# Performance work log

Measured on AMD Instinct MI355X. Metric: run time of the kernel, lower is better.

The kernel has to match this reference:

```python
import jax, jax.numpy as jnp
import numpy as np
import math

DIM = 2048
N_PHASES = 8
B, L = 4, 4096


def setup_inputs() -> dict:
    key = jax.random.key(0)
    ks = jax.random.split(key, 12)
    s = 0.02
    return {
        "x": jax.random.normal(ks[0], (B, L, DIM), dtype=jnp.float32),
        # weights stored [in, out] (transposed vs torch Linear)
        "Wp": jax.random.normal(ks[1], (DIM, N_PHASES), dtype=jnp.float32) * s,
        "bp": jnp.zeros((N_PHASES,), dtype=jnp.float32),
        "Wa": jax.random.normal(ks[2], (DIM, N_PHASES), dtype=jnp.float32) * s,
        "ba": jnp.zeros((N_PHASES,), dtype=jnp.float32),
        "Wv": jax.random.normal(ks[3], (DIM, DIM), dtype=jnp.float32) * s,
        "bv": jnp.zeros((DIM,), dtype=jnp.float32),
        "ln_g": jnp.ones((DIM,), dtype=jnp.float32),
        "ln_b": jnp.zeros((DIM,), dtype=jnp.float32),
        "Wo": jax.random.normal(ks[4], (DIM, DIM), dtype=jnp.float32) * s,
        "bo": jnp.zeros((DIM,), dtype=jnp.float32),
    }


def _layernorm(h, g, b, eps=1e-5):
    mu = jnp.mean(h, axis=-1, keepdims=True)
    var = jnp.var(h, axis=-1, keepdims=True)
    return (h - mu) * jax.lax.rsqrt(var + eps) * g + b


def reference(x, Wp, bp, Wa, ba, Wv, bv, ln_g, ln_b, Wo, bo):
    Llen = x.shape[1]
    phase = jnp.tanh(x @ Wp + bp) * math.pi          # [B,L,P]
    amp = jax.nn.softplus(x @ Wa + ba) + 0.1         # [B,L,P]
    value = x @ Wv + bv                              # [B,L,D]
    # (value[...,None,:] * cos_p[...,None] * amp[...,None]).sum(-2)
    # == value * sum_p(cos_p * amp)  -- algebraic factorization, same math.
    cr = jnp.sum(jnp.cos(phase) * amp, axis=-1, keepdims=True)  # [B,L,1]
    ci = jnp.sum(jnp.sin(phase) * amp, axis=-1, keepdims=True)  # [B,L,1]
    bound = value * (cr + ci)                        # real+imag combined
    retrieved = jnp.cumsum(bound, axis=1)            # [B,L,D]
    h = _layernorm(retrieved / math.sqrt(Llen), ln_g, ln_b)
    return x + h @ Wo + bo
```

## Files before the change

kernel.cpp:

```cpp
#include <hip/hip_runtime.h>

#define DIM   2048
#define LSEQ  4096
#define BATCH 4
#define NTOK  (BATCH*LSEQ)
#define NCH   16
#define CHL   (LSEQ/NCH)
#define PI_F  3.14159265358979f
#define NT    (DIM/64)

typedef __bf16 bf16x8 __attribute__((ext_vector_type(8)));
typedef float  f32x4  __attribute__((ext_vector_type(4)));
typedef float  f32x8  __attribute__((ext_vector_type(8)));
typedef unsigned short ushort8 __attribute__((ext_vector_type(8)));

__device__ __forceinline__ unsigned short f2bf(float f) {
    unsigned int u = __float_as_uint(f);
    u += 0x7fffu + ((u >> 16) & 1u);
    return (unsigned short)(u >> 16);
}

__device__ __forceinline__ void gload_lds16(const void* g, void* l) {
    __builtin_amdgcn_global_load_lds(
        (const __attribute__((address_space(1))) void*)g,
        (__attribute__((address_space(3))) void*)l, 16, 0, 0);
}

__global__ __launch_bounds__(256) void k_transpose(const float* __restrict__ src,
                                                   unsigned short* __restrict__ dst) {
    __shared__ float tile[32][33];
    int tx = threadIdx.x, ty = threadIdx.y;
    int k0 = blockIdx.y * 32, n0 = blockIdx.x * 32;
#pragma unroll
    for (int r = 0; r < 4; r++)
        tile[ty + r * 8][tx] = src[(size_t)(k0 + ty + r * 8) * DIM + n0 + tx];
    __syncthreads();
#pragma unroll
    for (int r = 0; r < 4; r++)
        dst[(size_t)(n0 + ty + r * 8) * DIM + k0 + tx] = f2bf(tile[tx][ty + r * 8]);
}

__global__ __launch_bounds__(256) void k_prep_wpa(const float* __restrict__ Wp,
                                                  const float* __restrict__ Wa,
                                                  unsigned short* __restrict__ WpaT) {
    int idx = blockIdx.x * 256 + threadIdx.x;
    int p = idx >> 11, k = idx & (DIM - 1);
    float v = (p < 8) ? Wp[(size_t)k * 8 + p] : Wa[(size_t)k * 8 + (p - 8)];
    WpaT[idx] = f2bf(v);
}

__global__ __launch_bounds__(256) void k_sproj_mfma(const float* __restrict__ x,
                                                    const unsigned short* __restrict__ WpaT,
                                                    const float* __restrict__ bp,
                                                    const float* __restrict__ ba,
                                                    float* __restrict__ s,
                                                    unsigned short* __restrict__ xbf) {
    const int t = threadIdx.x;
    const int w = t >> 6, l = t & 63;
    const int r16 = l & 15, q = l >> 4;
    const int rowbase = blockIdx.x * 64 + w * 16;
    const float* xr = x + (size_t)(rowbase + r16) * DIM + q * 8;
    unsigned short* xw = xbf + (size_t)(rowbase + r16) * DIM + q * 8;
    const unsigned short* wrow = WpaT + r16 * DIM + q * 8;

    f32x4 acc = {};
#pragma unroll 8
    for (int ks = 0; ks < 64; ks++) {
        f32x8 xv = *(const f32x8*)(xr + ks * 32);
        ushort8 xo;
#pragma unroll
        for (int j = 0; j < 8; j++) xo[j] = f2bf(xv[j]);
        *(ushort8*)(xw + ks * 32) = xo;
        bf16x8 av = *(const bf16x8*)&xo;
        bf16x8 bv = *(const bf16x8*)(wrow + ks * 32);
        acc = __builtin_amdgcn_mfma_f32_16x16x32_bf16(av, bv, acc, 0, 0, 0);
    }
    const float bpv = bp[r16 & 7], bav = ba[r16 & 7];
#pragma unroll
    for (int j = 0; j < 4; j++) {
        float z = acc[j];
        float zo = __shfl_xor(z, 8);
        float zp = z + bpv, za = zo + bav;
        float ph = tanhf(zp) * PI_F;
        float amp = (za > 20.f ? za : log1pf(expf(za))) + 0.1f;
        float term = (r16 < 8) ? (cosf(ph) + sinf(ph)) * amp : 0.f;
        term += __shfl_xor(term, 1);
        term += __shfl_xor(term, 2);
        term += __shfl_xor(term, 4);
        if (r16 == 0) s[rowbase + q * 4 + j] = term;
    }
}

__device__ __forceinline__ void stage_unit(const unsigned short* __restrict__ src,
                                           unsigned short* dst, int tid) {
    gload_lds16(src,                     dst + tid * 8);
    gload_lds16(src + (size_t)128 * DIM, dst + (tid + 512) * 8);
}

template <int EPI>
__global__ __launch_bounds__(512, 2) void k_gemm256(const unsigned short* __restrict__ A,
                                                    const unsigned short* __restrict__ Bt,
                                                    const float* __restrict__ bias,
                                                    const float* __restrict__ sc,
                                                    const float* __restrict__ resid,
                                                    float* __restrict__ C,
                                                    float* __restrict__ part) {
    __shared__ __align__(16) unsigned short As[2][2][256 * 32];
    __shared__ __align__(16) unsigned short Bs[2][2][256 * 32];
    __shared__ float colsum[2][256];
    const int tid = threadIdx.x;
    const int w = tid >> 6, lane = tid & 63;
    const int wm = w >> 2, wn = w & 3;
    const int r16 = lane & 15, q = lane >> 4;

    int bid = blockIdx.x;
    int wgs = (bid & 7) * 64 + (bid >> 3);
    int tm = wgs >> 3, tn = wgs & 7;
    int brow = tm * 256, bcol = tn * 256;

    const int kq = ((tid & 3) ^ ((tid >> 3) & 3)) * 8;
    const unsigned short* pA = A  + (size_t)(brow + (tid >> 2)) * DIM + kq;
    const unsigned short* pB = Bt + (size_t)(bcol + (tid >> 2)) * DIM + kq;

    const int qs8 = (q ^ ((r16 >> 1) & 3)) * 8;
    const int offA = (wm * 128 + r16) * 32 + qs8;
    const int offB = (wn * 64  + r16) * 32 + qs8;

    f32x4 acc[8][4] = {};

    stage_unit(pA,      &As[0][0][0], tid);
    stage_unit(pB,      &Bs[0][0][0], tid);
    stage_unit(pA + 32, &As[0][1][0], tid);
    stage_unit(pB + 32, &Bs[0][1][0], tid);
    stage_unit(pA + 64, &As[1][0][0], tid);
    asm volatile("s_waitcnt vmcnt(6)" ::: "memory");
    __builtin_amdgcn_s_barrier();

    for (int t = 0; t < NT; ++t) {
        const int s = t & 1;
        unsigned short* A0 = &As[s][0][0];
        unsigned short* A1 = &As[s][1][0];
        unsigned short* B0 = &Bs[s][0][0];
        unsigned short* B1 = &Bs[s][1][0];
        unsigned short* nA1 = &As[s ^ 1][1][0];
        unsigned short* nB0 = &Bs[s ^ 1][0][0];
        unsigned short* nB1 = &Bs[s ^ 1][1][0];
        const unsigned short* pAn = pA + (t + 1) * 64;
        const unsigned short* pBn = pB + (t + 1) * 64;

        bf16x8 aF[4], bF[4];
#pragma unroll
        for (int i = 0; i < 4; i++) aF[i] = *(const bf16x8*)(A0 + offA + i * 512);
#pragma unroll
        for (int i = 0; i < 4; i++) bF[i] = *(const bf16x8*)(B0 + offB + i * 512);
        stage_unit(pBn, nB0, tid);
        __builtin_amdgcn_s_barrier();
        __builtin_amdgcn_s_setprio(1);
#pragma unroll
        for (int i = 0; i < 4; i++)
#pragma unroll
            for (int n = 0; n < 4; n++)
                acc[i][n] = __builtin_amdgcn_mfma_f32_16x16x32_bf16(aF[i], bF[n], acc[i][n], 0, 0, 0);
        __builtin_amdgcn_s_setprio(0);
        __builtin_amdgcn_s_barrier();

#pragma unroll
        for (int i = 0; i < 4; i++) aF[i] = *(const bf16x8*)(A0 + offA + 2048 + i * 512);
        stage_unit(pAn + 32, nA1, tid);
        __builtin_amdgcn_s_barrier();
        __builtin_amdgcn_s_setprio(1);
#pragma unroll
        for (int i = 0; i < 4; i++)
#pragma unroll
            for (int n = 0; n < 4; n++)
                acc[4 + i][n] = __builtin_amdgcn_mfma_f32_16x16x32_bf16(aF[i], bF[n], acc[4 + i][n], 0, 0, 0);
        __builtin_amdgcn_s_setprio(0);
        asm volatile("s_waitcnt vmcnt(6)" ::: "memory");
        __builtin_amdgcn_s_barrier();

#pragma unroll
        for (int i = 0; i < 4; i++) aF[i] = *(const bf16x8*)(A1 + offA + i * 512);
#pragma unroll
        for (int i = 0; i < 4; i++) bF[i] = *(const bf16x8*)(B1 + offB + i * 512);
        stage_unit(pBn + 32, nB1, tid);
        __builtin_amdgcn_s_barrier();
        __builtin_amdgcn_s_setprio(1);
#pragma unroll
        for (int i = 0; i < 4; i++)
#pragma unroll
            for (int n = 0; n < 4; n++)
                acc[i][n] = __builtin_amdgcn_mfma_f32_16x16x32_bf16(aF[i], bF[n], acc[i][n], 0, 0, 0);
        __builtin_amdgcn_s_setprio(0);
        __builtin_amdgcn_s_barrier();

#pragma unroll
        for (int i = 0; i < 4; i++) aF[i] = *(const bf16x8*)(A1 + offA + 2048 + i * 512);
        stage_unit(pA + (t + 2) * 64, A0, tid);
        __builtin_amdgcn_s_barrier();
        __builtin_amdgcn_s_setprio(1);
#pragma unroll
        for (int i = 0; i < 4; i++)
#pragma unroll
            for (int n = 0; n < 4; n++)
                acc[4 + i][n] = __builtin_amdgcn_mfma_f32_16x16x32_bf16(aF[i], bF[n], acc[4 + i][n], 0, 0, 0);
        __builtin_amdgcn_s_setprio(0);
        asm volatile("s_waitcnt vmcnt(6)" ::: "memory");
        __builtin_amdgcn_s_barrier();
    }

    float cs[4] = {0.f, 0.f, 0.f, 0.f};
#pragma unroll
    for (int mf = 0; mf < 8; mf++) {
        int r0 = brow + wm * 128 + mf * 16 + q * 4;
#pragma unroll
        for (int nf = 0; nf < 4; nf++) {
            int c = bcol + wn * 64 + nf * 16 + r16;
            float bc = bias[c];
#pragma unroll
            for (int j = 0; j < 4; j++) {
                int r = r0 + j;
                float v = acc[mf][nf][j] + bc;
                if (EPI == 0) { v *= sc[r]; cs[nf] += v; }
                else          v += resid[(size_t)r * DIM + c];
                C[(size_t)r * DIM + c] = v;
            }
        }
    }
    if (EPI == 0) {
#pragma unroll
        for (int nf = 0; nf < 4; nf++) {
            float v = cs[nf];
            v += __shfl_xor(v, 16);
            v += __shfl_xor(v, 32);
            if (q == 0) colsum[wm][wn * 64 + nf * 16 + r16] = v;
        }
        __syncthreads();
        if (tid < 256)
            part[(size_t)(brow >> 8) * DIM + bcol + tid] = colsum[0][tid] + colsum[1][tid];
    }
}

__global__ __launch_bounds__(256) void k_scan_offsets(float* __restrict__ part) {
    int tid = blockIdx.x * 256 + threadIdx.x;
    int d = tid & (DIM - 1);
    int b = tid >> 11;
    float run = 0.f;
    for (int ch = 0; ch < NCH; ch++) {
        size_t idx = ((size_t)b * NCH + ch) * DIM + d;
        float v = part[idx];
        part[idx] = run;
        run += v;
    }
}

__global__ __launch_bounds__(256) void k_scan_apply(float* __restrict__ bound,
                                                    const float* __restrict__ part) {
    int tid = blockIdx.x * 256 + threadIdx.x;
    int d = tid & (DIM - 1);
    int ch = (tid >> 11) & (NCH - 1);
    int b = tid >> 15;
    float run = part[tid];
    float* p = bound + ((size_t)b * LSEQ + (size_t)ch * CHL) * DIM + d;
    for (int i = 0; i < CHL; i++) { run += p[(size_t)i * DIM]; p[(size_t)i * DIM] = run; }
}

__global__ __launch_bounds__(256) void k_lnorm(const float* __restrict__ ret,
                                               const float* __restrict__ g,
                                               const float* __restrict__ bta,
                                               unsigned short* __restrict__ h) {
    int row = blockIdx.x, t = threadIdx.x;
    const float4* r4 = (const float4*)(ret + (size_t)row * DIM);
    float4 v0 = r4[2 * t], v1 = r4[2 * t + 1];
    const float scl = 1.0f / 64.0f;
    v0.x *= scl; v0.y *= scl; v0.z *= scl; v0.w *= scl;
    v1.x *= scl; v1.y *= scl; v1.z *= scl; v1.w *= scl;
    float sum = v0.x + v0.y + v0.z + v0.w + v1.x + v1.y + v1.z + v1.w;
    float ss  = v0.x*v0.x + v0.y*v0.y + v0.z*v0.z + v0.w*v0.w
              + v1.x*v1.x + v1.y*v1.y + v1.z*v1.z + v1.w*v1.w;
#pragma unroll
    for (int off = 32; off; off >>= 1) { sum += __shfl_down(sum, off); ss += __shfl_down(ss, off); }
    __shared__ float red[4][2];
    __shared__ float mu_s, rstd_s;
    int w = t >> 6, lane = t & 63;
    if (lane == 0) { red[w][0] = sum; red[w][1] = ss; }
    __syncthreads();
    if (t == 0) {
        float S = red[0][0] + red[1][0] + red[2][0] + red[3][0];
        float Q = red[0][1] + red[1][1] + red[2][1] + red[3][1];
        float mu = S / DIM;
        float var = Q / DIM - mu * mu;
        mu_s = mu; rstd_s = rsqrtf(var + 1e-5f);
    }
    __syncthreads();
    float mu = mu_s, rstd = rstd_s;
    f32x8 gv = *(const f32x8*)(g + t * 8);
    f32x8 bv = *(const f32x8*)(bta + t * 8);
    float vv[8] = { v0.x, v0.y, v0.z, v0.w, v1.x, v1.y, v1.z, v1.w };
    ushort8 o;
#pragma unroll
    for (int j = 0; j < 8; j++) o[j] = f2bf((vv[j] - mu) * rstd * gv[j] + bv[j]);
    *(ushort8*)(h + (size_t)row * DIM + t * 8) = o;
}

extern "C" void kernel_launch(void* const* d_in, const int* in_sizes, int n_in,
                              void* d_out, int out_size, void* d_ws, size_t ws_size,
                              hipStream_t stream) {
    const float* x   = (const float*)d_in[0];
    const float* Wp  = (const float*)d_in[1];
    const float* bp  = (const float*)d_in[2];
    const float* Wa  = (const float*)d_in[3];
    const float* ba  = (const float*)d_in[4];
    const float* Wv  = (const float*)d_in[5];
    const float* bv  = (const float*)d_in[6];
    const float* lng = (const float*)d_in[7];
    const float* lnb = (const float*)d_in[8];
    const float* Wo  = (const float*)d_in[9];
    const float* bo  = (const float*)d_in[10];
    float* out = (float*)d_out;

    char* ws = (char*)d_ws;
    unsigned short* x_bf = (unsigned short*)ws; ws += (size_t)NTOK * DIM * 2;
    unsigned short* WvT  = (unsigned short*)ws; ws += (size_t)DIM * DIM * 2;
    unsigned short* WoT  = (unsigned short*)ws; ws += (size_t)DIM * DIM * 2;
    unsigned short* WpaT = (unsigned short*)ws; ws += (size_t)16 * DIM * 2;
    float* svec          = (float*)ws;          ws += (size_t)NTOK * 4;
    float* bound         = (float*)ws;          ws += (size_t)NTOK * DIM * 4;
    float* part          = (float*)ws;          ws += (size_t)BATCH * NCH * DIM * 4;

    dim3 tb(32, 8);
    k_transpose<<<dim3(64, 64), tb, 0, stream>>>(Wv, WvT);
    k_transpose<<<dim3(64, 64), tb, 0, stream>>>(Wo, WoT);
    k_prep_wpa<<<128, 256, 0, stream>>>(Wp, Wa, WpaT);
    k_sproj_mfma<<<NTOK / 64, 256, 0, stream>>>(x, WpaT, bp, ba, svec, x_bf);

    k_gemm256<0><<<512, 512, 0, stream>>>(x_bf, WvT, bv, svec, nullptr, bound, part);

    k_scan_offsets<<<BATCH * DIM / 256, 256, 0, stream>>>(part);
    k_scan_apply<<<BATCH * NCH * DIM / 256, 256, 0, stream>>>(bound, part);

    k_lnorm<<<NTOK, 256, 0, stream>>>(bound, lng, lnb, x_bf);

    k_gemm256<1><<<512, 512, 0, stream>>>(x_bf, WoT, bo, nullptr, x, out, nullptr);
}
```

Measured before the change: 433.5 us.

## Restructure GEMM main loop into two phases with fewer barriers

The bf16 MFMA GEMM main loop goes from four sub-phases, each with two barriers, to two phases per k-tile. Each phase loads all 8 A fragments and 4 B fragments, issues two staging loads, runs 32 MFMAs, then waits with vmcnt(4) and hits a single barrier. The aim is to cut barrier count and synchronisation stalls while giving the scheduler larger MFMA blocks, plus unroll-by-2 of the loop. In exchange it holds more fragment registers, which may lower occupancy, and the changed staging order and wait counts raise the risk of LDS read/write races.

```diff
diff --git a/kernel.cpp b/kernel.cpp
--- a/kernel.cpp
+++ b/kernel.cpp
@@ -136,75 +136,41 @@
     asm volatile("s_waitcnt vmcnt(6)" ::: "memory");
     __builtin_amdgcn_s_barrier();
 
+#pragma unroll 2
     for (int t = 0; t < NT; ++t) {
         const int s = t & 1;
-        unsigned short* A0 = &As[s][0][0];
-        unsigned short* A1 = &As[s][1][0];
-        unsigned short* B0 = &Bs[s][0][0];
-        unsigned short* B1 = &Bs[s][1][0];
-        unsigned short* nA1 = &As[s ^ 1][1][0];
-        unsigned short* nB0 = &Bs[s ^ 1][0][0];
-        unsigned short* nB1 = &Bs[s ^ 1][1][0];
-        const unsigned short* pAn = pA + (t + 1) * 64;
-        const unsigned short* pBn = pB + (t + 1) * 64;
-
-        bf16x8 aF[4], bF[4];
-#pragma unroll
-        for (int i = 0; i < 4; i++) aF[i] = *(const bf16x8*)(A0 + offA + i * 512);
-#pragma unroll
-        for (int i = 0; i < 4; i++) bF[i] = *(const bf16x8*)(B0 + offB + i * 512);
-        stage_unit(pBn, nB0, tid);
-        __builtin_amdgcn_s_barrier();
+        bf16x8 aF[8], bF[4];
+
+#pragma unroll
+        for (int i = 0; i < 8; i++) aF[i] = *(const bf16x8*)(&As[s][0][0] + offA + i * 512);
+#pragma unroll
+        for (int n = 0; n < 4; n++) bF[n] = *(const bf16x8*)(&Bs[s][0][0] + offB + n * 512);
+        stage_unit(pB + (t + 1) * 64,      &Bs[s ^ 1][0][0], tid);
+        stage_unit(pA + (t + 1) * 64 + 32, &As[s ^ 1][1][0], tid);
         __builtin_amdgcn_s_setprio(1);
 #pragma unroll
-        for (int i = 0; i < 4; i++)
+        for (int i = 0; i < 8; i++)
 #pragma unroll
             for (int n = 0; n < 4; n++)
                 acc[i][n] = __builtin_amdgcn_mfma_f32_16x16x32_bf16(aF[i], bF[n], acc[i][n], 0, 0, 0);
         __builtin_amdgcn_s_setprio(0);
+        asm volatile("s_waitcnt vmcnt(4)" ::: "memory");
         __builtin_amdgcn_s_barrier();
 
 #pragma unroll
-        for (int i = 0; i < 4; i++) aF[i] = *(const bf16x8*)(A0 + offA + 2048 + i * 512);
-        stage_unit(pAn + 32, nA1, tid);
-        __builtin_amdgcn_s_barrier();
+        for (int i = 0; i < 8; i++) aF[i] = *(const bf16x8*)(&As[s][1][0] + offA + i * 512);
+#pragma unroll
+        for (int n = 0; n < 4; n++) bF[n] = *(const bf16x8*)(&Bs[s][1][0] + offB + n * 512);
+        stage_unit(pB + (t + 1) * 64 + 32, &Bs[s ^ 1][1][0], tid);
+        stage_unit(pA + (t + 2) * 64,      &As[s][0][0], tid);
         __builtin_amdgcn_s_setprio(1);
 #pragma unroll
-        for (int i = 0; i < 4; i++)
-#pragma unroll
-            for (int n = 0; n < 4; n++)
-                acc[4 + i][n] = __builtin_amdgcn_mfma_f32_16x16x32_bf16(aF[i], bF[n], acc[4 + i][n], 0, 0, 0);
-        __builtin_amdgcn_s_setprio(0);
-        asm volatile("s_waitcnt vmcnt(6)" ::: "memory");
-        __builtin_amdgcn_s_barrier();
-
-#pragma unroll
-        for (int i = 0; i < 4; i++) aF[i] = *(const bf16x8*)(A1 + offA + i * 512);
-#pragma unroll
-        for (int i = 0; i < 4; i++) bF[i] = *(const bf16x8*)(B1 + offB + i * 512);
-        stage_unit(pBn + 32, nB1, tid);
-        __builtin_amdgcn_s_barrier();
-        __builtin_amdgcn_s_setprio(1);
-#pragma unroll
-        for (int i = 0; i < 4; i++)
+        for (int i = 0; i < 8; i++)
 #pragma unroll
             for (int n = 0; n < 4; n++)
                 acc[i][n] = __builtin_amdgcn_mfma_f32_16x16x32_bf16(aF[i], bF[n], acc[i][n], 0, 0, 0);
         __builtin_amdgcn_s_setprio(0);
-        __builtin_amdgcn_s_barrier();
-
-#pragma unroll
-        for (int i = 0; i < 4; i++) aF[i] = *(const bf16x8*)(A1 + offA + 2048 + i * 512);
-        stage_unit(pA + (t + 2) * 64, A0, tid);
-        __builtin_amdgcn_s_barrier();
-        __builtin_amdgcn_s_setprio(1);
-#pragma unroll
-        for (int i = 0; i < 4; i++)
-#pragma unroll
-            for (int n = 0; n < 4; n++)
-                acc[4 + i][n] = __builtin_amdgcn_mfma_f32_16x16x32_bf16(aF[i], bF[n], acc[4 + i][n], 0, 0, 0);
-        __builtin_amdgcn_s_setprio(0);
-        asm volatile("s_waitcnt vmcnt(6)" ::: "memory");
+        asm volatile("s_waitcnt vmcnt(4)" ::: "memory");
         __builtin_amdgcn_s_barrier();
     }
 
```

Result: slower. 450.8 us (+4.0%).

## Store cumsum intermediate in bf16 and read residual from bf16 copy of x

Applied to the files above, without the earlier changes.

The value-GEMM epilogue now writes the scaled bound tensor as bf16 instead of fp32. The scan and layernorm kernels read and write that bf16 buffer, still accumulating the running sum in fp32. The output GEMM reads the residual from the existing bf16 copy of x, and layernorm writes to a separate h buffer. This roughly halves the memory traffic of the bandwidth-bound scan, layernorm and residual passes, at the cost of bf16 rounding on the stored prefix sums and on the residual added to the output.

```diff
diff --git a/kernel.cpp b/kernel.cpp
--- a/kernel.cpp
+++ b/kernel.cpp
@@ -12,12 +12,16 @@
 typedef __bf16 bf16x8 __attribute__((ext_vector_type(8)));
 typedef float  f32x4  __attribute__((ext_vector_type(4)));
 typedef float  f32x8  __attribute__((ext_vector_type(8)));
+typedef unsigned short ushort4_t __attribute__((ext_vector_type(4)));
 typedef unsigned short ushort8 __attribute__((ext_vector_type(8)));
 
 __device__ __forceinline__ unsigned short f2bf(float f) {
     unsigned int u = __float_as_uint(f);
     u += 0x7fffu + ((u >> 16) & 1u);
     return (unsigned short)(u >> 16);
+}
+__device__ __forceinline__ float bf2f(unsigned short u) {
+    return __uint_as_float((unsigned int)u << 16);
 }
 
 __device__ __forceinline__ void gload_lds16(const void* g, void* l) {
@@ -102,8 +106,9 @@
                                                     const unsigned short* __restrict__ Bt,
                                                     const float* __restrict__ bias,
                                                     const float* __restrict__ sc,
-                                                    const float* __restrict__ resid,
+                                                    const unsigned short* __restrict__ residbf,
                                                     float* __restrict__ C,
+                                                    unsigned short* __restrict__ Cbf,
                                                     float* __restrict__ part) {
     __shared__ __align__(16) unsigned short As[2][2][256 * 32];
     __shared__ __align__(16) unsigned short Bs[2][2][256 * 32];
@@ -207,6 +212,7 @@
         asm volatile("s_waitcnt vmcnt(6)" ::: "memory");
         __builtin_amdgcn_s_barrier();
     }
+    asm volatile("s_waitcnt vmcnt(0)" ::: "memory");
 
     float cs[4] = {0.f, 0.f, 0.f, 0.f};
 #pragma unroll
@@ -220,9 +226,14 @@
             for (int j = 0; j < 4; j++) {
                 int r = r0 + j;
                 float v = acc[mf][nf][j] + bc;
-                if (EPI == 0) { v *= sc[r]; cs[nf] += v; }
-                else          v += resid[(size_t)r * DIM + c];
-                C[(size_t)r * DIM + c] = v;
+                if (EPI == 0) {
+                    v *= sc[r];
+                    cs[nf] += v;
+                    Cbf[(size_t)r * DIM + c] = f2bf(v);
+                } else {
+                    v += bf2f(residbf[(size_t)r * DIM + c]);
+                    C[(size_t)r * DIM + c] = v;
+                }
             }
         }
     }
@@ -253,30 +264,35 @@
     }
 }
 
-__global__ __launch_bounds__(256) void k_scan_apply(float* __restrict__ bound,
+__global__ __launch_bounds__(256) void k_scan_apply(unsigned short* __restrict__ boundbf,
                                                     const float* __restrict__ part) {
     int tid = blockIdx.x * 256 + threadIdx.x;
     int d = tid & (DIM - 1);
     int ch = (tid >> 11) & (NCH - 1);
     int b = tid >> 15;
     float run = part[tid];
-    float* p = bound + ((size_t)b * LSEQ + (size_t)ch * CHL) * DIM + d;
-    for (int i = 0; i < CHL; i++) { run += p[(size_t)i * DIM]; p[(size_t)i * DIM] = run; }
-}
-
-__global__ __launch_bounds__(256) void k_lnorm(const float* __restrict__ ret,
+    unsigned short* p = boundbf + ((size_t)b * LSEQ + (size_t)ch * CHL) * DIM + d;
+    for (int i = 0; i < CHL; i++) {
+        run += bf2f(p[(size_t)i * DIM]);
+        p[(size_t)i * DIM] = f2bf(run);
+    }
+}
+
+__global__ __launch_bounds__(256) void k_lnorm(const unsigned short* __restrict__ retbf,
                                                const float* __restrict__ g,
                                                const float* __restrict__ bta,
                                                unsigned short* __restrict__ h) {
     int row = blockIdx.x, t = threadIdx.x;
-    const float4* r4 = (const float4*)(ret + (size_t)row * DIM);
-    float4 v0 = r4[2 * t], v1 = r4[2 * t + 1];
+    ushort8 rv = *(const ushort8*)(retbf + (size_t)row * DIM + t * 8);
     const float scl = 1.0f / 64.0f;
-    v0.x *= scl; v0.y *= scl; v0.z *= scl; v0.w *= scl;
-    v1.x *= scl; v1.y *= scl; v1.z *= scl; v1.w *= scl;
-    float sum = v0.x + v0.y + v0.z + v0.w + v1.x + v1.y + v1.z + v1.w;
-    float ss  = v0.x*v0.x + v0.y*v0.y + v0.z*v0.z + v0.w*v0.w
-              + v1.x*v1.x + v1.y*v1.y + v1.z*v1.z + v1.w*v1.w;
+    float vv[8];
+    float sum = 0.f, ss = 0.f;
+#pragma unroll
+    for (int j = 0; j < 8; j++) {
+        vv[j] = bf2f(rv[j]) * scl;
+        sum += vv[j];
+        ss  += vv[j] * vv[j];
+    }
 #pragma unroll
     for (int off = 32; off; off >>= 1) { sum += __shfl_down(sum, off); ss += __shfl_down(ss, off); }
     __shared__ float red[4][2];
@@ -295,7 +311,6 @@
     float mu = mu_s, rstd = rstd_s;
     f32x8 gv = *(const f32x8*)(g + t * 8);
     f32x8 bv = *(const f32x8*)(bta + t * 8);
-    float vv[8] = { v0.x, v0.y, v0.z, v0.w, v1.x, v1.y, v1.z, v1.w };
     ushort8 o;
 #pragma unroll
     for (int j = 0; j < 8; j++) o[j] = f2bf((vv[j] - mu) * rstd * gv[j] + bv[j]);
@@ -319,13 +334,14 @@
     float* out = (float*)d_out;
 
     char* ws = (char*)d_ws;
-    unsigned short* x_bf = (unsigned short*)ws; ws += (size_t)NTOK * DIM * 2;
-    unsigned short* WvT  = (unsigned short*)ws; ws += (size_t)DIM * DIM * 2;
-    unsigned short* WoT  = (unsigned short*)ws; ws += (size_t)DIM * DIM * 2;
-    unsigned short* WpaT = (unsigned short*)ws; ws += (size_t)16 * DIM * 2;
-    float* svec          = (float*)ws;          ws += (size_t)NTOK * 4;
-    float* bound         = (float*)ws;          ws += (size_t)NTOK * DIM * 4;
-    float* part          = (float*)ws;          ws += (size_t)BATCH * NCH * DIM * 4;
+    unsigned short* x_bf  = (unsigned short*)ws; ws += (size_t)NTOK * DIM * 2;
+    unsigned short* h_bf  = (unsigned short*)ws; ws += (size_t)NTOK * DIM * 2;
+    unsigned short* WvT   = (unsigned short*)ws; ws += (size_t)DIM * DIM * 2;
+    unsigned short* WoT   = (unsigned short*)ws; ws += (size_t)DIM * DIM * 2;
+    unsigned short* WpaT  = (unsigned short*)ws; ws += (size_t)16 * DIM * 2;
+    float* svec           = (float*)ws;          ws += (size_t)NTOK * 4;
+    unsigned short* bound = (unsigned short*)ws; ws += (size_t)NTOK * DIM * 2;
+    float* part           = (float*)ws;          ws += (size_t)BATCH * NCH * DIM * 4;
 
     dim3 tb(32, 8);
     k_transpose<<<dim3(64, 64), tb, 0, stream>>>(Wv, WvT);
@@ -333,12 +349,12 @@
     k_prep_wpa<<<128, 256, 0, stream>>>(Wp, Wa, WpaT);
     k_sproj_mfma<<<NTOK / 64, 256, 0, stream>>>(x, WpaT, bp, ba, svec, x_bf);
 
-    k_gemm256<0><<<512, 512, 0, stream>>>(x_bf, WvT, bv, svec, nullptr, bound, part);
+    k_gemm256<0><<<512, 512, 0, stream>>>(x_bf, WvT, bv, svec, nullptr, nullptr, bound, part);
 
     k_scan_offsets<<<BATCH * DIM / 256, 256, 0, stream>>>(part);
     k_scan_apply<<<BATCH * NCH * DIM / 256, 256, 0, stream>>>(bound, part);
 
-    k_lnorm<<<NTOK, 256, 0, stream>>>(bound, lng, lnb, x_bf);
-
-    k_gemm256<1><<<512, 512, 0, stream>>>(x_bf, WoT, bo, nullptr, x, out, nullptr);
-}
+    k_lnorm<<<NTOK, 256, 0, stream>>>(bound, lng, lnb, h_bf);
+
+    k_gemm256<1><<<512, 512, 0, stream>>>(h_bf, WoT, bo, nullptr, x_bf, out, nullptr, nullptr);
+}
```

Result: faster. 401.4 us (-7.4%).
